# Optimization experiments

Hardware: AMD Instinct MI355X
Metric: run time of the kernel (lower is better)

The kernel has to match this reference:

```python
import jax, jax.numpy as jnp
import numpy as np

N = 50000   # nodes
E = 800000  # edges (avg degree 16)
H = 3       # attention heads
D_IN, D_HID, D_OUT = 256, 64, 10


def setup_inputs() -> dict:
    key = jax.random.key(0)
    ks = jax.random.split(key, 8)
    x = jax.random.normal(ks[0], (N, D_IN), dtype=jnp.float32)
    edge_index = jax.random.randint(ks[1], (2, E), 0, N, dtype=jnp.int64)
    W1 = jax.random.normal(ks[2], (H, D_IN, D_HID), dtype=jnp.float32) / np.sqrt(D_IN)
    a_src1 = jax.random.normal(ks[3], (H, D_HID), dtype=jnp.float32) / np.sqrt(D_HID)
    a_dst1 = jax.random.normal(ks[4], (H, D_HID), dtype=jnp.float32) / np.sqrt(D_HID)
    W2 = jax.random.normal(ks[5], (H, D_HID, D_OUT), dtype=jnp.float32) / np.sqrt(D_HID)
    a_src2 = jax.random.normal(ks[6], (H, D_OUT), dtype=jnp.float32) / np.sqrt(D_OUT)
    a_dst2 = jax.random.normal(ks[7], (H, D_OUT), dtype=jnp.float32) / np.sqrt(D_OUT)
    return {"x": x, "edge_index": edge_index, "W1": W1, "a_src1": a_src1,
            "a_dst1": a_dst1, "W2": W2, "a_src2": a_src2, "a_dst2": a_dst2}


def gat_layer(x, src, dst, W, a_s, a_d, n):
    # x: [N, Din]; W: [H, Din, Dout]; returns [N, Dout] (heads averaged)
    z = jnp.einsum('nd,hde->nhe', x, W)                     # [N, H, Dout]
    e_src = jnp.einsum('nhe,he->nh', z, a_s)[src]           # [E, H]
    e_dst = jnp.einsum('nhe,he->nh', z, a_d)[dst]           # [E, H]
    e = jax.nn.leaky_relu(e_src + e_dst, 0.2)               # [E, H]
    # numerically-stable softmax over incoming edges of each dst node
    m = jax.lax.stop_gradient(jax.ops.segment_max(e, dst, num_segments=n))
    ex = jnp.exp(e - m[dst])                                # [E, H]
    denom = jax.ops.segment_sum(ex, dst, num_segments=n)    # [N, H]
    alpha = ex / (denom[dst] + 1e-16)                       # [E, H]
    out = jax.ops.segment_sum(z[src] * alpha[:, :, None], dst, num_segments=n)
    return out.mean(axis=1)                                 # [N, Dout]


def reference(x, edge_index, W1, a_src1, a_dst1, W2, a_src2, a_dst2):
    n = x.shape[0]
    src, dst = edge_index[0], edge_index[1]
    # dropout layers are identity in eval/deterministic mode
    h = gat_layer(x, src, dst, W1, a_src1, a_dst1, n)
    h = jax.nn.elu(h)
    h = gat_layer(h, src, dst, W2, a_src2, a_dst2, n)
    return h, jax.nn.log_softmax(h, axis=1)
```

## Files before the change

### kernel.cpp

```cpp
#include <hip/hip_runtime.h>
#include <math.h>

#define DIN  256
#define DHID 64
#define NH   3
#define DOUT 10
#define CAP  64

typedef __attribute__((ext_vector_type(8))) short bf16x8;
typedef __attribute__((ext_vector_type(4))) float f32x4;

__device__ inline unsigned short f2bf(float f) {
    unsigned u = __builtin_bit_cast(unsigned, f);
    unsigned r = (u + 0x7FFFu + ((u >> 16) & 1u)) >> 16;
    return (unsigned short)r;
}
__device__ inline float bf2f(unsigned short s) {
    unsigned u = ((unsigned)s) << 16;
    return __builtin_bit_cast(float, u);
}
__device__ inline f32x4 cvt4(ushort4 z) {
    f32x4 r;
    r[0] = bf2f(z.x); r[1] = bf2f(z.y); r[2] = bf2f(z.z); r[3] = bf2f(z.w);
    return r;
}


__global__ __launch_bounds__(256) void repack_zero_kernel(const float* __restrict__ W1,
                                                          const float* __restrict__ W2,
                                                          unsigned short* __restrict__ W1p,
                                                          float* __restrict__ W2cat,
                                                          int* __restrict__ cursor, int N) {
    int bid = blockIdx.x;
    int tid = threadIdx.x;
    int nzb = (N + 255) >> 8;
    if (bid < 192) {
        int idx = bid * 256 + tid;
        int j = idx & 7, l = (idx >> 3) & 63, q = (idx >> 9) & 7, t = idx >> 12;
        int c = t * 16 + (l & 15);
        int k = q * 32 + (l >> 4) * 8 + j;
        int h = c >> 6, jj = c & 63;
        W1p[idx] = f2bf(W1[h * 16384 + k * 64 + jj]);
    } else if (bid < 192 + nzb) {
        int i = (bid - 192) * 256 + tid;
        if (i < N) cursor[i] = 0;
    } else {
        int idx = (bid - 192 - nzb) * 256 + tid;
        if (idx < 2048) {
            int kk = idx >> 5, c = idx & 31;
            float wv = 0.f;
            if (c < 30) {
                int h = c / 10, j = c % 10;
                wv = W2[(h * 64 + kk) * 10 + j];
            }
            W2cat[idx] = wv;
        }
    }
}


__global__ __launch_bounds__(128) void gemm1_scatter_kernel(const float* __restrict__ x,
                                                            const bf16x8* __restrict__ W1p,
                                                            const float* __restrict__ a_s,
                                                            const float* __restrict__ a_d,
                                                            unsigned short* __restrict__ z1bf,
                                                            float* __restrict__ s1,
                                                            float* __restrict__ d1, int n,
                                                            const int* __restrict__ src,
                                                            const int* __restrict__ dst,
                                                            int* __restrict__ cursor,
                                                            unsigned short* __restrict__ esrcp,
                                                            int E, int G) {
    __shared__ unsigned short Xs[32][272];
    if ((int)blockIdx.x >= G) {
        int i = (blockIdx.x - G) * 128 + threadIdx.x;
        if (i < E) {
            int d = dst[i];
            int s = src[i];
            int pos = atomicAdd(cursor + d, 1);
            if (pos < CAP) esrcp[d * CAP + pos] = (unsigned short)s;
        }
        return;
    }

    int tid = threadIdx.x;
    int w = tid >> 6, lane = tid & 63;
    int m = lane & 15, quad = lane >> 4;
    int n0 = blockIdx.x * 32;

    for (int i = tid; i < 2048; i += 128) {
        int r = i >> 6, c4 = i & 63;
        int nn = n0 + r;
        float4 a = (nn < n) ? *(const float4*)(x + (size_t)nn * 256 + c4 * 4)
                            : (float4){0.f, 0.f, 0.f, 0.f};
        ushort4 b;
        b.x = f2bf(a.x); b.y = f2bf(a.y); b.z = f2bf(a.z); b.w = f2bf(a.w);
        *(ushort4*)(&Xs[r][c4 * 4]) = b;
    }
    __syncthreads();

    int rloc = w * 16 + m;
    f32x4 acc[12];
    #pragma unroll
    for (int t = 0; t < 12; ++t) acc[t] = (f32x4){0.f, 0.f, 0.f, 0.f};
    #pragma unroll
    for (int q = 0; q < 8; ++q) {
        bf16x8 af = *(const bf16x8*)(&Xs[rloc][q * 32 + quad * 8]);
        #pragma unroll
        for (int t = 0; t < 12; ++t) {
            bf16x8 bfr = W1p[(t * 8 + q) * 64 + lane];
            acc[t] = __builtin_amdgcn_mfma_f32_16x16x32_bf16(af, bfr, acc[t], 0, 0, 0);
        }
    }
    __syncthreads();

    float as_r[12], ad_r[12];
    #pragma unroll
    for (int t = 0; t < 12; ++t) { as_r[t] = a_s[t * 16 + m]; ad_r[t] = a_d[t * 16 + m]; }

    #pragma unroll
    for (int reg = 0; reg < 4; ++reg) {
        int row_loc = w * 16 + quad * 4 + reg;
        int row_out = n0 + row_loc;
        bool ok = row_out < n;
        float ps[3] = {0.f, 0.f, 0.f}, pd[3] = {0.f, 0.f, 0.f};
        #pragma unroll
        for (int t = 0; t < 12; ++t) {
            float v = acc[t][reg];
            Xs[row_loc][t * 16 + m] = f2bf(v);
            ps[t >> 2] += v * as_r[t];
            pd[t >> 2] += v * ad_r[t];
        }
        #pragma unroll
        for (int h = 0; h < 3; ++h) {
            float s = ps[h], d = pd[h];
            #pragma unroll
            for (int msk = 1; msk < 16; msk <<= 1) {
                s += __shfl_xor(s, msk, 16);
                d += __shfl_xor(d, msk, 16);
            }
            if (ok && m == 0) { s1[row_out * 4 + h] = s; d1[row_out * 4 + h] = d; }
        }
    }
    __syncthreads();

    for (int i = tid; i < 1536; i += 128) {
        int r = i / 48, c4 = i % 48;
        int nn = n0 + r;
        if (nn < n)
            *(ushort4*)(z1bf + (size_t)nn * 192 + c4 * 4) = *(const ushort4*)(&Xs[r][c4 * 4]);
    }
}


__global__ __launch_bounds__(256) void agg1_gemm2_kernel(
        const int* __restrict__ cnts, const unsigned short* __restrict__ esrcp,
        const float* __restrict__ s1, const float* __restrict__ d1,
        const unsigned short* __restrict__ z1bf,
        const float* __restrict__ W2cat, const float* __restrict__ as2,
        const float* __restrict__ ad2,
        unsigned short* __restrict__ z2bf,
        float* __restrict__ s2, float* __restrict__ d2, int n) {
    __shared__ float Ws[64][32];
    __shared__ float wlds[4][196];
    __shared__ float hb[4][64];
    __shared__ float tb[4][64];
    int tid = threadIdx.x;
    int lane = tid & 63, wave = tid >> 6;

    for (int idx = tid; idx < 1024; idx += 256)
        ((float2*)&Ws[0][0])[idx] = ((const float2*)W2cat)[idx];
    __syncthreads();

    int v = blockIdx.x * 4 + wave;
    if (v >= n) return;
    int cnt = cnts[v]; if (cnt > CAP) cnt = CAP;
    int m16 = lane & 15;
    int grp = lane >> 4;
    int head = grp > 2 ? 2 : grp;
    bool rowact = lane < 48;
    float dv0 = d1[v * 4], dv1 = d1[v * 4 + 1], dv2 = d1[v * 4 + 2];
    float* wl = wlds[wave];

    int u_l = 0; float w0 = 0.f, w1 = 0.f, w2 = 0.f;
    if (lane < cnt) {
        u_l = (int)esrcp[v * CAP + lane];
        float4 sv = *(const float4*)(s1 + (size_t)u_l * 4);
        float e0 = sv.x + dv0; e0 = e0 > 0.f ? e0 : 0.2f * e0;
        float e1 = sv.y + dv1; e1 = e1 > 0.f ? e1 : 0.2f * e1;
        float e2 = sv.z + dv2; e2 = e2 > 0.f ? e2 : 0.2f * e2;
        w0 = __expf(e0); w1 = __expf(e1); w2 = __expf(e2);
    }
    wl[lane] = w0; wl[65 + lane] = w1; wl[130 + lane] = w2;

    f32x4 acc = (f32x4){0.f, 0.f, 0.f, 0.f};
    if (rowact) {
        int rnd = (cnt + 7) & ~7;
        const int wb = head * 65;
        ushort4 zr[8]; float wr[8];
        #pragma unroll
        for (int i = 0; i < 8; ++i) {
            int u = __builtin_amdgcn_readlane(u_l, i);
            zr[i] = *(const ushort4*)(z1bf + (size_t)u * 192 + lane * 4);
            wr[i] = wl[wb + i];
        }
        for (int j = 8; j < rnd; j += 8) {
            ushort4 zn[8]; float wn[8];
            #pragma unroll
            for (int i = 0; i < 8; ++i) {
                int u = __builtin_amdgcn_readlane(u_l, j + i);
                zn[i] = *(const ushort4*)(z1bf + (size_t)u * 192 + lane * 4);
                wn[i] = wl[wb + j + i];
            }
            #pragma unroll
            for (int i = 0; i < 8; ++i) acc += cvt4(zr[i]) * wr[i];
            #pragma unroll
            for (int i = 0; i < 8; ++i) { zr[i] = zn[i]; wr[i] = wn[i]; }
        }
        #pragma unroll
        for (int i = 0; i < 8; ++i) acc += cvt4(zr[i]) * wr[i];
    }

    float4 wv4 = *(const float4*)(&wl[head * 65 + m16 * 4]);
    float denp = wv4.x + wv4.y + wv4.z + wv4.w;
    #pragma unroll
    for (int msk = 1; msk < 16; msk <<= 1) denp += __shfl_xor(denp, msk, 16);

    float invd = (1.f / 3.f) / (denp + 1e-16f);
    float acc0 = rowact ? acc[0] * invd : 0.f;
    float acc1 = rowact ? acc[1] * invd : 0.f;
    float acc2 = rowact ? acc[2] * invd : 0.f;
    float acc3 = rowact ? acc[3] * invd : 0.f;
    acc0 += __shfl_down(acc0, 32, 64); acc0 += __shfl_down(acc0, 16, 64);
    acc1 += __shfl_down(acc1, 32, 64); acc1 += __shfl_down(acc1, 16, 64);
    acc2 += __shfl_down(acc2, 32, 64); acc2 += __shfl_down(acc2, 16, 64);
    acc3 += __shfl_down(acc3, 32, 64); acc3 += __shfl_down(acc3, 16, 64);
    if (lane < 16) {
        float4 o;
        o.x = acc0 > 0.f ? acc0 : __expf(acc0) - 1.f;
        o.y = acc1 > 0.f ? acc1 : __expf(acc1) - 1.f;
        o.z = acc2 > 0.f ? acc2 : __expf(acc2) - 1.f;
        o.w = acc3 > 0.f ? acc3 : __expf(acc3) - 1.f;
        *(float4*)(&hb[wave][lane * 4]) = o;
    }

    int c = lane & 31, half = lane >> 5;
    int k0 = half * 32;
    float zc0 = 0.f, zc1 = 0.f;
    #pragma unroll
    for (int k = 0; k < 32; k += 2) {
        zc0 += hb[wave][k0 + k]     * Ws[k0 + k][c];
        zc1 += hb[wave][k0 + k + 1] * Ws[k0 + k + 1][c];
    }
    float zc = zc0 + zc1;
    zc += __shfl_down(zc, 32, 64);
    if (lane < 32) {
        z2bf[(size_t)v * 32 + c] = f2bf(zc);
        if (c < 30) {
            tb[wave][c]      = zc * as2[c];
            tb[wave][32 + c] = zc * ad2[c];
        }
    }
    if (lane < 6) {
        int h = lane >> 1;
        int base = (lane & 1) * 32 + h * 10;
        float sum = 0.f;
        #pragma unroll
        for (int j = 0; j < 10; ++j) sum += tb[wave][base + j];
        if ((lane & 1) == 0) s2[v * 4 + h] = sum;
        else                 d2[v * 4 + h] = sum;
    }
}


__global__ __launch_bounds__(256) void agg2_kernel(const int* __restrict__ cnts,
                                                   const unsigned short* __restrict__ esrcp,
                                                   const float* __restrict__ s2,
                                                   const float* __restrict__ d2,
                                                   const unsigned short* __restrict__ z2bf,
                                                   float* __restrict__ out, int n) {
    __shared__ float wlds[4][196];
    __shared__ float dlds[4][4];
    int tid = threadIdx.x;
    int lane = tid & 63, wave = tid >> 6;
    int v = blockIdx.x * 4 + wave;
    if (v >= n) return;
    int cnt = cnts[v]; if (cnt > CAP) cnt = CAP;
    int c2 = lane & 15;
    int quad = lane >> 4;
    int headc = c2 < 5 ? 0 : (c2 < 10 ? 1 : 2);
    int headg = quad > 2 ? 2 : quad;
    float dv0 = d2[v * 4], dv1 = d2[v * 4 + 1], dv2 = d2[v * 4 + 2];
    float* wl = wlds[wave];

    int u_l = 0; float w0 = 0.f, w1 = 0.f, w2 = 0.f;
    if (lane < cnt) {
        u_l = (int)esrcp[v * CAP + lane];
        float4 sv = *(const float4*)(s2 + (size_t)u_l * 4);
        float e0 = sv.x + dv0; e0 = e0 > 0.f ? e0 : 0.2f * e0;
        float e1 = sv.y + dv1; e1 = e1 > 0.f ? e1 : 0.2f * e1;
        float e2 = sv.z + dv2; e2 = e2 > 0.f ? e2 : 0.2f * e2;
        w0 = __expf(e0); w1 = __expf(e1); w2 = __expf(e2);
    }
    wl[lane] = w0; wl[65 + lane] = w1; wl[130 + lane] = w2;

    float ax = 0.f, ay = 0.f;
    {
        int rnd = (cnt + 7) & ~7;
        const int wb = headc * 65;
        int ua = __shfl(u_l, quad, 64);
        int ub = __shfl(u_l, 4 + quad, 64);
        float wa = wl[wb + quad], wbb = wl[wb + 4 + quad];
        ushort2 za = *(const ushort2*)(z2bf + (size_t)ua * 32 + c2 * 2);
        ushort2 zb = *(const ushort2*)(z2bf + (size_t)ub * 32 + c2 * 2);
        for (int j = 8; j < rnd; j += 8) {
            int un1 = __shfl(u_l, j + quad, 64);
            int un2 = __shfl(u_l, j + 4 + quad, 64);
            float wn1 = wl[wb + j + quad], wn2 = wl[wb + j + 4 + quad];
            ushort2 zn1 = *(const ushort2*)(z2bf + (size_t)un1 * 32 + c2 * 2);
            ushort2 zn2 = *(const ushort2*)(z2bf + (size_t)un2 * 32 + c2 * 2);
            ax += wa * bf2f(za.x) + wbb * bf2f(zb.x);
            ay += wa * bf2f(za.y) + wbb * bf2f(zb.y);
            wa = wn1; wbb = wn2; za = zn1; zb = zn2;
        }
        ax += wa * bf2f(za.x) + wbb * bf2f(zb.x);
        ay += wa * bf2f(za.y) + wbb * bf2f(zb.y);
    }

    float4 wv = *(const float4*)(&wl[headg * 65 + c2 * 4]);
    float denp = wv.x + wv.y + wv.z + wv.w;
    #pragma unroll
    for (int msk = 1; msk < 16; msk <<= 1) denp += __shfl_xor(denp, msk, 16);
    if (c2 == 0 && quad < 3) dlds[wave][quad] = denp;
    float den = dlds[wave][headc];

    ax += __shfl_down(ax, 32, 64); ax += __shfl_down(ax, 16, 64);
    ay += __shfl_down(ay, 32, 64); ay += __shfl_down(ay, 16, 64);
    float inv = 1.f / (den + 1e-16f);
    float rx = ax * inv, ry = ay * inv;
    float rx5  = __shfl(rx, lane + 5, 64);
    float rx10 = __shfl(rx, lane + 10, 64);
    float ry5  = __shfl(ry, lane + 5, 64);
    float ry10 = __shfl(ry, lane + 10, 64);
    float rrx = (rx + rx5 + rx10) * (1.f / 3.f);
    float rry = (ry + ry5 + ry10) * (1.f / 3.f);
    bool act = lane < 5;
    float mx = act ? fmaxf(rrx, rry) : -1e30f;
    #pragma unroll
    for (int msk = 1; msk < 8; msk <<= 1) mx = fmaxf(mx, __shfl_xor(mx, msk, 8));
    float e = act ? (__expf(rrx - mx) + __expf(rry - mx)) : 0.f;
    #pragma unroll
    for (int msk = 1; msk < 8; msk <<= 1) e += __shfl_xor(e, msk, 8);
    float lg = __logf(e);
    if (act) {
        float2 o1; o1.x = rrx; o1.y = rry;
        float2 o2; o2.x = rrx - mx - lg; o2.y = rry - mx - lg;
        *(float2*)(out + (size_t)v * DOUT + c2 * 2) = o1;
        *(float2*)(out + (size_t)n * DOUT + (size_t)v * DOUT + c2 * 2) = o2;
    }
}


extern "C" void kernel_launch(void* const* d_in, const int* in_sizes, int n_in,
                              void* d_out, int out_size, void* d_ws, size_t ws_size,
                              hipStream_t stream) {
    const float* x   = (const float*)d_in[0];
    const int*   ei  = (const int*)d_in[1];
    const float* W1  = (const float*)d_in[2];
    const float* as1 = (const float*)d_in[3];
    const float* ad1 = (const float*)d_in[4];
    const float* W2  = (const float*)d_in[5];
    const float* as2 = (const float*)d_in[6];
    const float* ad2 = (const float*)d_in[7];
    float* out = (float*)d_out;

    const int N = in_sizes[0] / DIN;
    const int E = in_sizes[1] / 2;
    const int* src = ei;
    const int* dst = ei + E;

    char* p = (char*)d_ws;
    auto alloc = [&](size_t bytes) -> void* {
        void* r = (void*)p;
        p += (bytes + 255) & ~(size_t)255;
        return r;
    };
    int* cursor  = (int*)alloc((size_t)N * 4);
    unsigned short* esrcp = (unsigned short*)alloc((size_t)N * CAP * 2);
    unsigned short* W1p  = (unsigned short*)alloc((size_t)49152 * 2);
    float* W2cat = (float*)alloc((size_t)2048 * 4);
    unsigned short* z1bf = (unsigned short*)alloc((size_t)N * 192 * 2);
    float* s1    = (float*)alloc((size_t)N * 4 * 4);
    float* d1    = (float*)alloc((size_t)N * 4 * 4);
    unsigned short* z2bf = (unsigned short*)alloc((size_t)N * 32 * 2);
    float* s2    = (float*)alloc((size_t)N * 4 * 4);
    float* d2    = (float*)alloc((size_t)N * 4 * 4);
    (void)alloc(512);

    int nzb = (N + 255) / 256;
    repack_zero_kernel<<<192 + nzb + 8, 256, 0, stream>>>(W1, W2, W1p, W2cat, cursor, N);

    int G = (N + 31) / 32;
    int S = (E + 127) / 128;
    gemm1_scatter_kernel<<<G + S, 128, 0, stream>>>(x, (const bf16x8*)W1p, as1, ad1,
                                                    z1bf, s1, d1, N,
                                                    src, dst, cursor, esrcp, E, G);

    agg1_gemm2_kernel<<<(N + 3) / 4, 256, 0, stream>>>(cursor, esrcp, s1, d1, z1bf,
                                                       W2cat, as2, ad2, z2bf, s2, d2, N);
    agg2_kernel<<<(N + 3) / 4, 256, 0, stream>>>(cursor, esrcp, s2, d2, z2bf, out, N);
}
```

Baseline: 262.5 us.

## Split edge scatter into partitioned kernel separate from GEMM1

Moves the edge-to-CSR scatter out of the fused GEMM1 kernel into its own launch. Blocks are assigned a chunk of 2048 edges plus one of 8 destination-node partitions, and each block handles only the edges whose destination falls in its partition, the aim being to keep atomics and writes within an L2/XCD-local region. The cost is that every edge is read 8 times, and the scatter no longer overlaps with the GEMM inside one launch.

```diff
diff --git a/kernel.cpp b/kernel.cpp
--- a/kernel.cpp
+++ b/kernel.cpp
@@ -59,30 +59,40 @@
 }
 
 
-__global__ __launch_bounds__(128) void gemm1_scatter_kernel(const float* __restrict__ x,
-                                                            const bf16x8* __restrict__ W1p,
-                                                            const float* __restrict__ a_s,
-                                                            const float* __restrict__ a_d,
-                                                            unsigned short* __restrict__ z1bf,
-                                                            float* __restrict__ s1,
-                                                            float* __restrict__ d1, int n,
-                                                            const int* __restrict__ src,
-                                                            const int* __restrict__ dst,
-                                                            int* __restrict__ cursor,
-                                                            unsigned short* __restrict__ esrcp,
-                                                            int E, int G) {
-    __shared__ unsigned short Xs[32][272];
-    if ((int)blockIdx.x >= G) {
-        int i = (blockIdx.x - G) * 128 + threadIdx.x;
+#define SCHUNK 2048
+
+__global__ __launch_bounds__(256) void scatter_kernel(const int* __restrict__ src,
+                                                      const int* __restrict__ dst,
+                                                      int* __restrict__ cursor,
+                                                      unsigned short* __restrict__ esrcp,
+                                                      int E, int pbase) {
+    int part = blockIdx.x & 7;
+    int base = (blockIdx.x >> 3) * SCHUNK;
+    int tid = threadIdx.x;
+    int lo = part * pbase, hi = lo + pbase;
+    #pragma unroll
+    for (int k = 0; k < SCHUNK / 256; ++k) {
+        int i = base + k * 256 + tid;
         if (i < E) {
             int d = dst[i];
             int s = src[i];
-            int pos = atomicAdd(cursor + d, 1);
-            if (pos < CAP) esrcp[d * CAP + pos] = (unsigned short)s;
-        }
-        return;
-    }
-
+            if (d >= lo && d < hi) {
+                int pos = atomicAdd(cursor + d, 1);
+                if (pos < CAP) esrcp[d * CAP + pos] = (unsigned short)s;
+            }
+        }
+    }
+}
+
+
+__global__ __launch_bounds__(128) void gemm1_mfma_kernel(const float* __restrict__ x,
+                                                         const bf16x8* __restrict__ W1p,
+                                                         const float* __restrict__ a_s,
+                                                         const float* __restrict__ a_d,
+                                                         unsigned short* __restrict__ z1bf,
+                                                         float* __restrict__ s1,
+                                                         float* __restrict__ d1, int n) {
+    __shared__ unsigned short Xs[32][272];
     int tid = threadIdx.x;
     int w = tid >> 6, lane = tid & 63;
     int m = lane & 15, quad = lane >> 4;
@@ -400,12 +410,12 @@
     int nzb = (N + 255) / 256;
     repack_zero_kernel<<<192 + nzb + 8, 256, 0, stream>>>(W1, W2, W1p, W2cat, cursor, N);
 
-    int G = (N + 31) / 32;
-    int S = (E + 127) / 128;
-    gemm1_scatter_kernel<<<G + S, 128, 0, stream>>>(x, (const bf16x8*)W1p, as1, ad1,
-                                                    z1bf, s1, d1, N,
-                                                    src, dst, cursor, esrcp, E, G);
-
+    int pbase = (N + 7) / 8;
+    int nchunks = (E + SCHUNK - 1) / SCHUNK;
+    scatter_kernel<<<nchunks * 8, 256, 0, stream>>>(src, dst, cursor, esrcp, E, pbase);
+
+    gemm1_mfma_kernel<<<(N + 31) / 32, 128, 0, stream>>>(x, (const bf16x8*)W1p, as1, ad1,
+                                                         z1bf, s1, d1, N);
     agg1_gemm2_kernel<<<(N + 3) / 4, 256, 0, stream>>>(cursor, esrcp, s1, d1, z1bf,
                                                        W2cat, as2, ad2, z2bf, s2, d2, N);
     agg2_kernel<<<(N + 3) / 4, 256, 0, stream>>>(cursor, esrcp, s2, d2, z2bf, out, N);
```

Result: faster. 248.6 us (-5.3%).
